# Performance work log

Hardware: AMD Instinct MI355X
Metric: run time of the kernel (lower is better)

## Reference

```python
import jax, jax.numpy as jnp
import numpy as np

INPUT_DIM = 512
KEY_DIM = 256
VOCAB = 10000
MAX_LEN = 300


def setup_inputs() -> dict:
    key = jax.random.key(0)
    ks = jax.random.split(key, 20)
    s = 0.05
    B, S, D, K, V = 32, 196, INPUT_DIM, KEY_DIM, VOCAB
    inp = {
        'x': jax.random.normal(ks[0], (B, S, D), jnp.float32),
        'emb': jax.random.normal(ks[1], (V, D), jnp.float32) * s,
        'Wk': jax.random.normal(ks[2], (K, D), jnp.float32) * s,
        'bk': jnp.zeros((K,), jnp.float32),
        'Wv': jax.random.normal(ks[3], (K, D), jnp.float32) * s,
        'bv': jnp.zeros((K,), jnp.float32),
        'Wq': jax.random.normal(ks[4], (K, D), jnp.float32) * s,
        'bq': jnp.zeros((K,), jnp.float32),
        'Wp': jax.random.normal(ks[5], (V, D + K), jnp.float32) * s,
        'bp': jnp.zeros((V,), jnp.float32),
        # LSTM cell 0: input = concat(embed, context) -> D + K
        'Wih0': jax.random.normal(ks[6], (4 * D, D + K), jnp.float32) * s,
        'Whh0': jax.random.normal(ks[7], (4 * D, D), jnp.float32) * s,
        'bih0': jnp.zeros((4 * D,), jnp.float32),
        'bhh0': jnp.zeros((4 * D,), jnp.float32),
        # LSTM cell 1: input = hidden of cell 0 -> D
        'Wih1': jax.random.normal(ks[8], (4 * D, D), jnp.float32) * s,
        'Whh1': jax.random.normal(ks[9], (4 * D, D), jnp.float32) * s,
        'bih1': jnp.zeros((4 * D,), jnp.float32),
        'bhh1': jnp.zeros((4 * D,), jnp.float32),
    }
    return inp


def _lstm_cell(inp, h, c, Wih, Whh, bih, bhh):
    # torch LSTMCell gate order: i, f, g, o
    gates = inp @ Wih.T + bih + h @ Whh.T + bhh
    i, f, g, o = jnp.split(gates, 4, axis=-1)
    c_new = jax.nn.sigmoid(f) * c + jax.nn.sigmoid(i) * jnp.tanh(g)
    h_new = jax.nn.sigmoid(o) * jnp.tanh(c_new)
    return h_new, c_new


def reference(x, emb, Wk, bk, Wv, bv, Wq, bq, Wp, bp,
              Wih0, Whh0, bih0, bhh0, Wih1, Whh1, bih1, bhh1):
    B = x.shape[0]
    D = Whh0.shape[1]
    K = Wk.shape[0]
    scale = 1.0 / jnp.sqrt(jnp.asarray(K, x.dtype))
    keys = x @ Wk.T + bk      # (B, S, K)
    values = x @ Wv.T + bv    # (B, S, K)

    tok0 = jnp.zeros((B,), jnp.int32)           # argmax of zeros(B,1) == 0
    ctx0 = jnp.zeros((B, K), x.dtype)
    h0 = jnp.zeros((B, D), x.dtype)
    c0 = jnp.zeros((B, D), x.dtype)
    h1 = jnp.zeros((B, D), x.dtype)
    c1 = jnp.zeros((B, D), x.dtype)

    def step(carry, _):
        tok, ctx, h0, c0, h1, c1 = carry
        embed = jnp.concatenate([emb[tok], ctx], axis=1)   # (B, D+K)
        h0, c0 = _lstm_cell(embed, h0, c0, Wih0, Whh0, bih0, bhh0)
        h1, c1 = _lstm_cell(h0, h1, c1, Wih1, Whh1, bih1, bhh1)
        q = h1 @ Wq.T + bq                                  # (B, K)
        energy = jnp.einsum('bsk,bk->bs', keys, q) * scale  # (B, S)
        attn = jax.nn.softmax(energy, axis=-1)
        ctx = jnp.einsum('bs,bsk->bk', attn, values)        # (B, K)
        out = jnp.concatenate([h1, ctx], axis=1)            # (B, D+K)
        pred = out @ Wp.T + bp                              # (B, V)
        tok = jnp.argmax(pred, axis=-1).astype(jnp.int32)
        return (tok, ctx, h0, c0, h1, c1), pred

    _, preds = jax.lax.scan(step, (tok0, ctx0, h0, c0, h1, c1), None, length=MAX_LEN)
    return jnp.transpose(preds, (1, 0, 2))  # (B, MAX_LEN, V)
```

## Files before the change

kernel.cpp:

```cpp
#include <hip/hip_runtime.h>
#include <math.h>


typedef unsigned long long u64;

#define NS 196
#define ND 512
#define NK 256
#define NV 10000
#define NT 300
#define NBLK 256
#define NTHR 512
#define NPRED 209
#define ATT0 224
#define SCOPE __HIP_MEMORY_SCOPE_AGENT

__device__ __forceinline__ float sigm(float x) { return 1.0f / (1.0f + expf(-x)); }

__device__ __forceinline__ float aldf(const float* p) {
  return __hip_atomic_load(p, __ATOMIC_RELAXED, SCOPE);
}
__device__ __forceinline__ void astf(float* p, float v) {
  __hip_atomic_store(p, v, __ATOMIC_RELAXED, SCOPE);
}
__device__ __forceinline__ u64 aldu(const u64* p) {
  return __hip_atomic_load(p, __ATOMIC_RELAXED, SCOPE);
}
__device__ __forceinline__ void astu(u64* p, u64 v) {
  __hip_atomic_store(p, v, __ATOMIC_RELAXED, SCOPE);
}

__device__ __forceinline__ u64 packmax(float x, int v) {
  unsigned u = __float_as_uint(x);
  u = (u & 0x80000000u) ? ~u : (u | 0x80000000u);
  return ((u64)u << 32) | (u64)(0xFFFFFFFFu - (unsigned)v);
}

__device__ __forceinline__ int eslot(int b, int k4) {
  return b * 32 + ((k4 & ~7) | ((k4 ^ b) & 7));
}

__device__ __forceinline__ void gbar(unsigned* bar, int bid, unsigned ep, bool fenced) {
  __syncthreads();
  if (threadIdx.x == 0) {
    if (fenced) __threadfence();
    asm volatile("s_waitcnt vmcnt(0)" ::: "memory");
    const int g = bid & 7;
    const unsigned old = __hip_atomic_fetch_add(&bar[g * 32], 1u, __ATOMIC_RELAXED, SCOPE);
    if (old == ep * 32u - 1u) {
      const unsigned r = __hip_atomic_fetch_add(&bar[512], 1u, __ATOMIC_RELAXED, SCOPE);
      if (r == ep * 8u - 1u) {
#pragma unroll
        for (int i = 0; i < 8; ++i)
          __hip_atomic_store(&bar[256 + i * 32], ep, __ATOMIC_RELAXED, SCOPE);
      }
    }
    while (__hip_atomic_load(&bar[256 + g * 32], __ATOMIC_RELAXED, SCOPE) < ep)
      __builtin_amdgcn_s_sleep(1);
    if (fenced) __threadfence();
  }
  __syncthreads();
}

__global__ __launch_bounds__(256) void k_zbar(unsigned* bar) {
  const int i = blockIdx.x * 256 + threadIdx.x;
  if (i < 1024) bar[i] = 0u;
}

struct Params {
  const float *x, *emb, *Wk, *bk, *Wv, *bv, *Wq, *bq, *Wp, *bp;
  const float *Wih0, *Whh0, *bih0, *bhh0, *Wih1, *Whh1, *bih1, *bhh1;
  float *out, *keys, *values, *h0t, *h1t, *c0, *c1, *ctx;
  u64 *amax;
  unsigned *bar;
};

__global__ __launch_bounds__(NTHR, 1) void k_all(Params p) {
  extern __shared__ float dyn[];
  float* W0lds = dyn;
  float* W1lds = dyn + 10240;
  float* stage = dyn + 18432;

  __shared__ __align__(16) float arena[2560];
  __shared__ int tok_lds[32];
  __shared__ u64 cand2[32][12];

  const int bid = blockIdx.x;
  const int t = threadIdx.x;
  const int lane = t & 63;
  const int w = t >> 6;

#define GP(ks, r, b)  arena[((ks) * 8 + (r)) * 32 + (b)]
#define GS(r, b)      arena[1024 + (r) * 32 + (b)]

  {
    const int g = bid * NTHR + t;
    if (g < 65536) astf(&p.h0t[g], 0.0f);
    if (g < 8192) astf(&p.ctx[g], 0.0f);
    if (g < 256) astu(&p.amax[g], (g < 32) ? ((1ull << 32) | 0xFFFFFFFFull) : 0ull);
  }
  if (t < 64) {
    const int idx = (bid * 2 + (t >> 5)) * 32 + (t & 31);
    p.c0[idx] = 0.0f;
    p.c1[idx] = 0.0f;
  }
  {
    const int r = t >> 6, ln = t & 63;
    const int grow = (r >> 1) * ND + bid * 2 + (r & 1);
    const float* s0i = p.Wih0 + (size_t)grow * 768;
    const float* s0h = p.Whh0 + (size_t)grow * ND;
#pragma unroll
    for (int j = 0; j < 5; ++j) {
      const int col = 4 * (ln + 64 * j);
      const float4 v = (col < 768) ? *(const float4*)(s0i + col)
                                   : *(const float4*)(s0h + (col - 768));
      *(float4*)(W0lds + r * 1280 + col) = v;
    }
    const float* s1i = p.Wih1 + (size_t)grow * ND;
    const float* s1h = p.Whh1 + (size_t)grow * ND;
#pragma unroll
    for (int j = 0; j < 4; ++j) {
      const int col = 4 * (ln + 64 * j);
      const float4 v = (col < 512) ? *(const float4*)(s1i + col)
                                   : *(const float4*)(s1h + (col - 512));
      *(float4*)(W1lds + r * 1024 + col) = v;
    }
  }
  {
    const int kc = bid & 7, bb = bid >> 3;
    const int kl = t & 31, sg = t >> 5;
    const int k = kc * 32 + kl;
    float ak[13], av[13];
#pragma unroll
    for (int i = 0; i < 13; ++i) { ak[i] = 0.f; av[i] = 0.f; }
    const float* wkr = p.Wk + (size_t)k * ND;
    const float* wvr = p.Wv + (size_t)k * ND;
    const float* xb = p.x + (size_t)bb * NS * ND;
    for (int j = 0; j < ND; j += 4) {
      const float4 wk4 = *(const float4*)(wkr + j);
      const float4 wv4 = *(const float4*)(wvr + j);
#pragma unroll
      for (int si = 0; si < 13; ++si) {
        const int s = sg + si * 16;
        if (s < NS) {
          const float4 xv = *(const float4*)(xb + (size_t)s * ND + j);
          ak[si] += wk4.x * xv.x + wk4.y * xv.y + wk4.z * xv.z + wk4.w * xv.w;
          av[si] += wv4.x * xv.x + wv4.y * xv.y + wv4.z * xv.z + wv4.w * xv.w;
        }
      }
    }
    const float bkk = p.bk[k], bvv = p.bv[k];
#pragma unroll
    for (int si = 0; si < 13; ++si) {
      const int s = sg + si * 16;
      if (s < NS) {
        const size_t o = ((size_t)bb * NS + s) * NK + k;
        p.keys[o] = ak[si] + bkk;
        p.values[o] = av[si] + bvv;
      }
    }
  }
  unsigned ep = 1;
  gbar(p.bar, bid, ep++, true);

  for (int step = 0; step < NT; ++step) {
    const int cur = step & 1;
    const float* h0c = p.h0t + cur * 16384;
    float* h0n = p.h0t + (cur ^ 1) * 16384;
    const float* h1c = p.h1t + cur * 16384;
    float* h1n = p.h1t + (cur ^ 1) * 16384;

    if (t < 32) {
      u64 m = aldu(&p.amax[t]);
#pragma unroll
      for (int s2 = 1; s2 < 8; ++s2) { const u64 o = aldu(&p.amax[s2 * 32 + t]); if (o > m) m = o; }
      tok_lds[t] = (int)(0xFFFFFFFFu - (unsigned)(m & 0xFFFFFFFFull));
    }
    __syncthreads();
    {
      const int rq = w >> 2, ks = w & 3;
      const int b = lane & 31, kq = lane >> 5;
      const int s8 = ks * 2 + kq;
      const int rb = rq * 4;
      float a0 = 0.f, a1 = 0.f, a2 = 0.f, a3 = 0.f;
      for (int c = 0; c < 4; ++c) {
        {
          const int eb = t >> 4, sl = t & 15;
          const float* er = p.emb + (size_t)tok_lds[eb] * ND + c * 128;
          *(float4*)(stage + 4 * eslot(eb, sl)) = *(const float4*)(er + 4 * sl);
          *(float4*)(stage + 4 * eslot(eb, sl + 16)) = *(const float4*)(er + 4 * (sl + 16));
        }
        __syncthreads();
#pragma unroll
        for (int jj = 0; jj < 4; ++jj) {
          const int f4 = ks * 8 + kq * 4 + jj;
          const float4 a4 = *(const float4*)(stage + 4 * eslot(b, f4));
          const int wc = c * 128 + 4 * f4;
          const float4 q0 = *(const float4*)(W0lds + (rb + 0) * 1280 + wc);
          const float4 q1 = *(const float4*)(W0lds + (rb + 1) * 1280 + wc);
          const float4 q2 = *(const float4*)(W0lds + (rb + 2) * 1280 + wc);
          const float4 q3 = *(const float4*)(W0lds + (rb + 3) * 1280 + wc);
          a0 += q0.x * a4.x + q0.y * a4.y + q0.z * a4.z + q0.w * a4.w;
          a1 += q1.x * a4.x + q1.y * a4.y + q1.z * a4.z + q1.w * a4.w;
          a2 += q2.x * a4.x + q2.y * a4.y + q2.z * a4.z + q2.w * a4.w;
          a3 += q3.x * a4.x + q3.y * a4.y + q3.z * a4.z + q3.w * a4.w;
        }
        __syncthreads();
      }
#pragma unroll 4
      for (int j = 0; j < 8; ++j) {
        const int k0 = (s8 * 8 + j) * 4;
        float4 x4;
        x4.x = aldf(p.ctx + (k0 + 0) * 32 + b);
        x4.y = aldf(p.ctx + (k0 + 1) * 32 + b);
        x4.z = aldf(p.ctx + (k0 + 2) * 32 + b);
        x4.w = aldf(p.ctx + (k0 + 3) * 32 + b);
        const int wc = 512 + k0;
        const float4 q0 = *(const float4*)(W0lds + (rb + 0) * 1280 + wc);
        const float4 q1 = *(const float4*)(W0lds + (rb + 1) * 1280 + wc);
        const float4 q2 = *(const float4*)(W0lds + (rb + 2) * 1280 + wc);
        const float4 q3 = *(const float4*)(W0lds + (rb + 3) * 1280 + wc);
        a0 += q0.x * x4.x + q0.y * x4.y + q0.z * x4.z + q0.w * x4.w;
        a1 += q1.x * x4.x + q1.y * x4.y + q1.z * x4.z + q1.w * x4.w;
        a2 += q2.x * x4.x + q2.y * x4.y + q2.z * x4.z + q2.w * x4.w;
        a3 += q3.x * x4.x + q3.y * x4.y + q3.z * x4.z + q3.w * x4.w;
      }
#pragma unroll 4
      for (int j = 0; j < 16; ++j) {
        const int k0 = (s8 * 16 + j) * 4;
        float4 x4;
        x4.x = aldf(h0c + (k0 + 0) * 32 + b);
        x4.y = aldf(h0c + (k0 + 1) * 32 + b);
        x4.z = aldf(h0c + (k0 + 2) * 32 + b);
        x4.w = aldf(h0c + (k0 + 3) * 32 + b);
        const int wc = 768 + k0;
        const float4 q0 = *(const float4*)(W0lds + (rb + 0) * 1280 + wc);
        const float4 q1 = *(const float4*)(W0lds + (rb + 1) * 1280 + wc);
        const float4 q2 = *(const float4*)(W0lds + (rb + 2) * 1280 + wc);
        const float4 q3 = *(const float4*)(W0lds + (rb + 3) * 1280 + wc);
        a0 += q0.x * x4.x + q0.y * x4.y + q0.z * x4.z + q0.w * x4.w;
        a1 += q1.x * x4.x + q1.y * x4.y + q1.z * x4.z + q1.w * x4.w;
        a2 += q2.x * x4.x + q2.y * x4.y + q2.z * x4.z + q2.w * x4.w;
        a3 += q3.x * x4.x + q3.y * x4.y + q3.z * x4.z + q3.w * x4.w;
      }
      a0 += __shfl_xor(a0, 32);
      a1 += __shfl_xor(a1, 32);
      a2 += __shfl_xor(a2, 32);
      a3 += __shfl_xor(a3, 32);
      if (kq == 0) {
        GP(ks, rb + 0, b) = a0; GP(ks, rb + 1, b) = a1;
        GP(ks, rb + 2, b) = a2; GP(ks, rb + 3, b) = a3;
      }
    }
    __syncthreads();
    if (t < 256) {
      const int r = t >> 5, b2 = t & 31;
      const int grow = (r >> 1) * ND + bid * 2 + (r & 1);
      GS(r, b2) = GP(0, r, b2) + GP(1, r, b2) + GP(2, r, b2) + GP(3, r, b2)
                + p.bih0[grow] + p.bhh0[grow];
    }
    __syncthreads();
    if (t < 64) {
      const int dl = t >> 5, b2 = t & 31;
      const int idx = (bid * 2 + dl) * 32 + b2;
      const float gi = GS(0 + dl, b2), gf = GS(2 + dl, b2);
      const float gg = GS(4 + dl, b2), go = GS(6 + dl, b2);
      const float cn = sigm(gf) * p.c0[idx] + sigm(gi) * tanhf(gg);
      p.c0[idx] = cn;
      astf(&h0n[idx], sigm(go) * tanhf(cn));
    }
    gbar(p.bar, bid, ep++, false);

    if (bid == 0 && t < 256) astu(&p.amax[t], 0ull);
    {
      const int rq = w >> 2, ks = w & 3;
      const int b = lane & 31, kq = lane >> 5;
      const int s8 = ks * 2 + kq;
      const int rb = rq * 4;
      float a0 = 0.f, a1 = 0.f, a2 = 0.f, a3 = 0.f;
#pragma unroll 4
      for (int j = 0; j < 32; ++j) {
        const int k0 = s8 * 128 + j * 4;
        const float* src = (k0 < 512) ? (h0n + k0 * 32) : (h1c + (k0 - 512) * 32);
        float4 x4;
        x4.x = aldf(src + 0 * 32 + b);
        x4.y = aldf(src + 1 * 32 + b);
        x4.z = aldf(src + 2 * 32 + b);
        x4.w = aldf(src + 3 * 32 + b);
        const float4 q0 = *(const float4*)(W1lds + (rb + 0) * 1024 + k0);
        const float4 q1 = *(const float4*)(W1lds + (rb + 1) * 1024 + k0);
        const float4 q2 = *(const float4*)(W1lds + (rb + 2) * 1024 + k0);
        const float4 q3 = *(const float4*)(W1lds + (rb + 3) * 1024 + k0);
        a0 += q0.x * x4.x + q0.y * x4.y + q0.z * x4.z + q0.w * x4.w;
        a1 += q1.x * x4.x + q1.y * x4.y + q1.z * x4.z + q1.w * x4.w;
        a2 += q2.x * x4.x + q2.y * x4.y + q2.z * x4.z + q2.w * x4.w;
        a3 += q3.x * x4.x + q3.y * x4.y + q3.z * x4.z + q3.w * x4.w;
      }
      a0 += __shfl_xor(a0, 32);
      a1 += __shfl_xor(a1, 32);
      a2 += __shfl_xor(a2, 32);
      a3 += __shfl_xor(a3, 32);
      if (kq == 0) {
        GP(ks, rb + 0, b) = a0; GP(ks, rb + 1, b) = a1;
        GP(ks, rb + 2, b) = a2; GP(ks, rb + 3, b) = a3;
      }
    }
    __syncthreads();
    if (t < 256) {
      const int r = t >> 5, b2 = t & 31;
      const int grow = (r >> 1) * ND + bid * 2 + (r & 1);
      GS(r, b2) = GP(0, r, b2) + GP(1, r, b2) + GP(2, r, b2) + GP(3, r, b2)
                + p.bih1[grow] + p.bhh1[grow];
    }
    __syncthreads();
    if (t < 64) {
      const int dl = t >> 5, b2 = t & 31;
      const int idx = (bid * 2 + dl) * 32 + b2;
      const float gi = GS(0 + dl, b2), gf = GS(2 + dl, b2);
      const float gg = GS(4 + dl, b2), go = GS(6 + dl, b2);
      const float cn = sigm(gf) * p.c1[idx] + sigm(gi) * tanhf(gg);
      p.c1[idx] = cn;
      astf(&h1n[idx], sigm(go) * tanhf(cn));
    }
    gbar(p.bar, bid, ep++, false);

    float acc[6];
#pragma unroll
    for (int r = 0; r < 6; ++r) acc[r] = 0.f;
    if (bid >= ATT0) {
      const int b = bid - ATT0;
      float* hb  = arena;
      float* qs  = arena + 512;
      float* red = arena + 768;
      float* smx = arena + 1024;
      hb[t] = aldf(h1n + t * 32 + b);
      __syncthreads();
      const int kl = lane & 31, rh = lane >> 5;
      for (int pp = 0; pp < 16; ++pp) {
        const int r = w * 32 + pp * 2 + rh;
        const float* wq = p.Wq + (size_t)r * ND + kl * 4;
        float a = 0.f;
#pragma unroll
        for (int i = 0; i < 4; ++i) {
          const float4 w4 = *(const float4*)(wq + i * 128);
          const float4 h4 = *(const float4*)(hb + i * 128 + kl * 4);
          a += w4.x * h4.x + w4.y * h4.y + w4.z * h4.z + w4.w * h4.w;
        }
#pragma unroll
        for (int mk = 1; mk < 32; mk <<= 1) a += __shfl_xor(a, mk);
        if (kl == 0) qs[r] = (a + p.bq[r]) * 0.0625f;
      }
      __syncthreads();
      for (int pp = 0; pp < 13; ++pp) {
        const int s = pp * 16 + w * 2 + rh;
        float a = 0.f;
        if (s < NS) {
          const float* kr = p.keys + ((size_t)b * NS + s) * NK + kl * 4;
#pragma unroll
          for (int i = 0; i < 2; ++i) {
            const float4 k4 = *(const float4*)(kr + i * 128);
            const float4 q4 = *(const float4*)(qs + i * 128 + kl * 4);
            a += k4.x * q4.x + k4.y * q4.y + k4.z * q4.z + k4.w * q4.w;
          }
        }
#pragma unroll
        for (int mk = 1; mk < 32; mk <<= 1) a += __shfl_xor(a, mk);
        if (kl == 0 && s < NS) smx[s] = a;
      }
      __syncthreads();
      float e = -INFINITY;
      if (t < 256) { e = (t < NS) ? smx[t] : -INFINITY; red[t] = e; }
      __syncthreads();
      for (int off = 128; off; off >>= 1) {
        if (t < off) red[t] = fmaxf(red[t], red[t + off]);
        __syncthreads();
      }
      const float mx = red[0];
      __syncthreads();
      float a = 0.f;
      if (t < 256) { a = (t < NS) ? expf(e - mx) : 0.f; red[t] = a; }
      __syncthreads();
      for (int off = 128; off; off >>= 1) {
        if (t < off) red[t] += red[t + off];
        __syncthreads();
      }
      const float inv = 1.0f / red[0];
      if (t < 256) smx[t] = a * inv;
      __syncthreads();
      if (t < 256) {
        const float* vb = p.values + (size_t)b * NS * NK + t;
        float c0_ = 0.f, c1_ = 0.f, c2_ = 0.f, c3_ = 0.f;
        for (int s = 0; s < NS; s += 4) {
          c0_ += smx[s + 0] * vb[(size_t)(s + 0) * NK];
          c1_ += smx[s + 1] * vb[(size_t)(s + 1) * NK];
          c2_ += smx[s + 2] * vb[(size_t)(s + 2) * NK];
          c3_ += smx[s + 3] * vb[(size_t)(s + 3) * NK];
        }
        astf(&p.ctx[t * 32 + b], (c0_ + c1_) + (c2_ + c3_));
      }
    } else if (bid < NPRED) {
      const int b = lane & 31, kq = lane >> 5;
      const int rbase = bid * 48 + w * 6;
      int rc[6];
#pragma unroll
      for (int r = 0; r < 6; ++r) rc[r] = (rbase + r < NV) ? (rbase + r) : (NV - 1);
#pragma unroll 2
      for (int j = 0; j < 64; ++j) {
        const int k0 = kq * 256 + j * 4;
        float4 x4;
        x4.x = aldf(h1n + (k0 + 0) * 32 + b);
        x4.y = aldf(h1n + (k0 + 1) * 32 + b);
        x4.z = aldf(h1n + (k0 + 2) * 32 + b);
        x4.w = aldf(h1n + (k0 + 3) * 32 + b);
#pragma unroll
        for (int r = 0; r < 6; ++r) {
          const float4 w4 = *(const float4*)(p.Wp + (size_t)rc[r] * 768 + k0);
          acc[r] += w4.x * x4.x + w4.y * x4.y + w4.z * x4.z + w4.w * x4.w;
        }
      }
    }
    gbar(p.bar, bid, ep++, false);

    if (bid < NPRED) {
      const int b = lane & 31, kq = lane >> 5;
      const int rbase = bid * 48 + w * 6;
      int rc[6];
#pragma unroll
      for (int r = 0; r < 6; ++r) rc[r] = (rbase + r < NV) ? (rbase + r) : (NV - 1);
#pragma unroll 2
      for (int j = 0; j < 32; ++j) {
        const int kc_ = kq * 128 + j * 4;
        float4 x4;
        x4.x = aldf(p.ctx + (kc_ + 0) * 32 + b);
        x4.y = aldf(p.ctx + (kc_ + 1) * 32 + b);
        x4.z = aldf(p.ctx + (kc_ + 2) * 32 + b);
        x4.w = aldf(p.ctx + (kc_ + 3) * 32 + b);
#pragma unroll
        for (int r = 0; r < 6; ++r) {
          const float4 w4 = *(const float4*)(p.Wp + (size_t)rc[r] * 768 + 512 + kc_);
          acc[r] += w4.x * x4.x + w4.y * x4.y + w4.z * x4.z + w4.w * x4.w;
        }
      }
#pragma unroll
      for (int r = 0; r < 6; ++r) acc[r] += __shfl_xor(acc[r], 32);
      if (kq == 0) {
#pragma unroll
        for (int r = 0; r < 6; ++r)
          arena[(w * 6 + r) * 32 + b] = acc[r];
      }
      __syncthreads();
      if (t < 384) {
        const int b2 = t & 31, rg = t >> 5;
        const int vb = bid * 48 + rg * 4;
        u64 m = 0ull;
        if (vb + 3 < NV) {
          float4 v;
          float* vp = &v.x;
#pragma unroll
          for (int i = 0; i < 4; ++i) {
            const int row = rg * 4 + i;
            vp[i] = arena[row * 32 + b2] + p.bp[vb + i];
          }
          *(float4*)(p.out + ((size_t)b2 * NT + step) * NV + vb) = v;
          m = packmax(v.x, vb + 0);
          const u64 o1 = packmax(v.y, vb + 1); if (o1 > m) m = o1;
          const u64 o2 = packmax(v.z, vb + 2); if (o2 > m) m = o2;
          const u64 o3 = packmax(v.w, vb + 3); if (o3 > m) m = o3;
        }
        cand2[b2][rg] = m;
      }
      __syncthreads();
      if (t < 32) {
        u64 mm = cand2[t][0];
#pragma unroll
        for (int i = 1; i < 12; ++i) { const u64 o = cand2[t][i]; if (o > mm) mm = o; }
        (void)__hip_atomic_fetch_max(&p.amax[(bid & 7) * 32 + t], mm, __ATOMIC_RELAXED, SCOPE);
      }
    }
    gbar(p.bar, bid, ep++, false);
  }
#undef GP
#undef GS
}

extern "C" void kernel_launch(void* const* d_in, const int* in_sizes, int n_in,
                              void* d_out, int out_size, void* d_ws, size_t ws_size,
                              hipStream_t stream) {
  (void)in_sizes; (void)n_in; (void)out_size; (void)ws_size;
  Params prm;
  prm.x    = (const float*)d_in[0];
  prm.emb  = (const float*)d_in[1];
  prm.Wk   = (const float*)d_in[2];
  prm.bk   = (const float*)d_in[3];
  prm.Wv   = (const float*)d_in[4];
  prm.bv   = (const float*)d_in[5];
  prm.Wq   = (const float*)d_in[6];
  prm.bq   = (const float*)d_in[7];
  prm.Wp   = (const float*)d_in[8];
  prm.bp   = (const float*)d_in[9];
  prm.Wih0 = (const float*)d_in[10];
  prm.Whh0 = (const float*)d_in[11];
  prm.bih0 = (const float*)d_in[12];
  prm.bhh0 = (const float*)d_in[13];
  prm.Wih1 = (const float*)d_in[14];
  prm.Whh1 = (const float*)d_in[15];
  prm.bih1 = (const float*)d_in[16];
  prm.bhh1 = (const float*)d_in[17];
  prm.out  = (float*)d_out;

  float* ws = (float*)d_ws;
  prm.keys   = ws;
  prm.values = prm.keys + 1605632;
  prm.h0t    = prm.values + 1605632;
  prm.h1t    = prm.h0t + 32768;
  prm.c0     = prm.h1t + 32768;
  prm.c1     = prm.c0 + 16384;
  prm.ctx    = prm.c1 + 16384;
  prm.amax   = (u64*)(prm.ctx + 8192);
  prm.bar    = (unsigned*)(prm.amax + 256);

  const int LDS = (10240 + 8192 + 4096) * 4;
  (void)hipFuncSetAttribute((const void*)k_all, hipFuncAttributeMaxDynamicSharedMemorySize, LDS);

  k_zbar<<<4, 256, 0, stream>>>(prm.bar);
  void* args[] = { &prm };
  (void)hipLaunchCooperativeKernel((const void*)k_all, dim3(NBLK), dim3(NTHR), args,
                                   (unsigned)LDS, stream);
}
```

Baseline: 24.84 ms.

## Vectorize recurrent-state loads with batch-major lane mapping in LSTM and projection matvecs

Remaps the threads of the LSTM0 ctx/h0 matvec, the LSTM1 matvec and the output projection so each lane loads four consecutive batch entries as one 16-byte volatile vector load. This replaces the scalar per-element atomic loads of the shared hidden and context state. Each lane now keeps v4f accumulators over four batches, and a three-level shuffle-xor reduction runs across the k-slices. The split of the LSTM0 work changes as well: the ctx/h0 part gets its own partial-sum region in the arena. In return the code needs more shuffles and more accumulator registers, and relies on volatile loads for visibility between blocks.

```diff
diff --git a/kernel.cpp b/kernel.cpp
--- a/kernel.cpp
+++ b/kernel.cpp
@@ -3,6 +3,7 @@
 
 
 typedef unsigned long long u64;
+typedef float v4f __attribute__((ext_vector_type(4)));
 
 #define NS 196
 #define ND 512
@@ -29,6 +30,9 @@
 __device__ __forceinline__ void astu(u64* p, u64 v) {
   __hip_atomic_store(p, v, __ATOMIC_RELAXED, SCOPE);
 }
+__device__ __forceinline__ v4f vald4(const float* p) {
+  return *(const volatile v4f*)p;
+}
 
 __device__ __forceinline__ u64 packmax(float x, int v) {
   unsigned u = __float_as_uint(x);
@@ -89,9 +93,6 @@
   const int t = threadIdx.x;
   const int lane = t & 63;
   const int w = t >> 6;
-
-#define GP(ks, r, b)  arena[((ks) * 8 + (r)) * 32 + (b)]
-#define GS(r, b)      arena[1024 + (r) * 32 + (b)]
 
   {
     const int g = bid * NTHR + t;
@@ -180,7 +181,6 @@
     {
       const int rq = w >> 2, ks = w & 3;
       const int b = lane & 31, kq = lane >> 5;
-      const int s8 = ks * 2 + kq;
       const int rb = rq * 4;
       float a0 = 0.f, a1 = 0.f, a2 = 0.f, a3 = 0.f;
       for (int c = 0; c < 4; ++c) {
@@ -207,64 +207,70 @@
         }
         __syncthreads();
       }
-#pragma unroll 4
-      for (int j = 0; j < 8; ++j) {
-        const int k0 = (s8 * 8 + j) * 4;
-        float4 x4;
-        x4.x = aldf(p.ctx + (k0 + 0) * 32 + b);
-        x4.y = aldf(p.ctx + (k0 + 1) * 32 + b);
-        x4.z = aldf(p.ctx + (k0 + 2) * 32 + b);
-        x4.w = aldf(p.ctx + (k0 + 3) * 32 + b);
-        const int wc = 512 + k0;
-        const float4 q0 = *(const float4*)(W0lds + (rb + 0) * 1280 + wc);
-        const float4 q1 = *(const float4*)(W0lds + (rb + 1) * 1280 + wc);
-        const float4 q2 = *(const float4*)(W0lds + (rb + 2) * 1280 + wc);
-        const float4 q3 = *(const float4*)(W0lds + (rb + 3) * 1280 + wc);
-        a0 += q0.x * x4.x + q0.y * x4.y + q0.z * x4.z + q0.w * x4.w;
-        a1 += q1.x * x4.x + q1.y * x4.y + q1.z * x4.z + q1.w * x4.w;
-        a2 += q2.x * x4.x + q2.y * x4.y + q2.z * x4.z + q2.w * x4.w;
-        a3 += q3.x * x4.x + q3.y * x4.y + q3.z * x4.z + q3.w * x4.w;
-      }
-#pragma unroll 4
-      for (int j = 0; j < 16; ++j) {
-        const int k0 = (s8 * 16 + j) * 4;
-        float4 x4;
-        x4.x = aldf(h0c + (k0 + 0) * 32 + b);
-        x4.y = aldf(h0c + (k0 + 1) * 32 + b);
-        x4.z = aldf(h0c + (k0 + 2) * 32 + b);
-        x4.w = aldf(h0c + (k0 + 3) * 32 + b);
-        const int wc = 768 + k0;
-        const float4 q0 = *(const float4*)(W0lds + (rb + 0) * 1280 + wc);
-        const float4 q1 = *(const float4*)(W0lds + (rb + 1) * 1280 + wc);
-        const float4 q2 = *(const float4*)(W0lds + (rb + 2) * 1280 + wc);
-        const float4 q3 = *(const float4*)(W0lds + (rb + 3) * 1280 + wc);
-        a0 += q0.x * x4.x + q0.y * x4.y + q0.z * x4.z + q0.w * x4.w;
-        a1 += q1.x * x4.x + q1.y * x4.y + q1.z * x4.z + q1.w * x4.w;
-        a2 += q2.x * x4.x + q2.y * x4.y + q2.z * x4.z + q2.w * x4.w;
-        a3 += q3.x * x4.x + q3.y * x4.y + q3.z * x4.z + q3.w * x4.w;
-      }
       a0 += __shfl_xor(a0, 32);
       a1 += __shfl_xor(a1, 32);
       a2 += __shfl_xor(a2, 32);
       a3 += __shfl_xor(a3, 32);
       if (kq == 0) {
-        GP(ks, rb + 0, b) = a0; GP(ks, rb + 1, b) = a1;
-        GP(ks, rb + 2, b) = a2; GP(ks, rb + 3, b) = a3;
+        arena[(ks * 8 + rb + 0) * 32 + b] = a0;
+        arena[(ks * 8 + rb + 1) * 32 + b] = a1;
+        arena[(ks * 8 + rb + 2) * 32 + b] = a2;
+        arena[(ks * 8 + rb + 3) * 32 + b] = a3;
+      }
+    }
+    {
+      const int rq4 = w >> 1, kh = w & 1;
+      const int bq = lane & 7, kl = lane >> 3;
+      const int r0 = rq4 * 2, r1 = r0 + 1;
+      const float* wr0 = W0lds + r0 * 1280 + 512 + kh * 384 + kl * 4;
+      const float* wr1 = W0lds + r1 * 1280 + 512 + kh * 384 + kl * 4;
+      v4f ac0 = {0.f, 0.f, 0.f, 0.f}, ac1 = {0.f, 0.f, 0.f, 0.f};
+#pragma unroll 3
+      for (int j = 0; j < 12; ++j) {
+        const int kk = kh * 384 + j * 32 + kl * 4;
+        const float* asrc = (kk < 256) ? (p.ctx + (size_t)kk * 32)
+                                       : (h0c + (size_t)(kk - 256) * 32);
+        const v4f x0 = vald4(asrc + 0 * 32 + bq * 4);
+        const v4f x1 = vald4(asrc + 1 * 32 + bq * 4);
+        const v4f x2 = vald4(asrc + 2 * 32 + bq * 4);
+        const v4f x3 = vald4(asrc + 3 * 32 + bq * 4);
+        const v4f q0 = *(const v4f*)(wr0 + j * 32);
+        const v4f q1 = *(const v4f*)(wr1 + j * 32);
+        ac0 += q0[0] * x0 + q0[1] * x1 + q0[2] * x2 + q0[3] * x3;
+        ac1 += q1[0] * x0 + q1[1] * x1 + q1[2] * x2 + q1[3] * x3;
+      }
+#pragma unroll
+      for (int c = 0; c < 4; ++c) {
+        float v0 = ac0[c], v1 = ac1[c];
+        v0 += __shfl_xor(v0, 8);  v1 += __shfl_xor(v1, 8);
+        v0 += __shfl_xor(v0, 16); v1 += __shfl_xor(v1, 16);
+        v0 += __shfl_xor(v0, 32); v1 += __shfl_xor(v1, 32);
+        ac0[c] = v0; ac1[c] = v1;
+      }
+      if (kl == 0) {
+#pragma unroll
+        for (int i = 0; i < 4; ++i) {
+          arena[1024 + (kh * 8 + r0) * 32 + bq * 4 + i] = ac0[i];
+          arena[1024 + (kh * 8 + r1) * 32 + bq * 4 + i] = ac1[i];
+        }
       }
     }
     __syncthreads();
     if (t < 256) {
       const int r = t >> 5, b2 = t & 31;
       const int grow = (r >> 1) * ND + bid * 2 + (r & 1);
-      GS(r, b2) = GP(0, r, b2) + GP(1, r, b2) + GP(2, r, b2) + GP(3, r, b2)
-                + p.bih0[grow] + p.bhh0[grow];
+      arena[1536 + r * 32 + b2] =
+          arena[(0 * 8 + r) * 32 + b2] + arena[(1 * 8 + r) * 32 + b2]
+        + arena[(2 * 8 + r) * 32 + b2] + arena[(3 * 8 + r) * 32 + b2]
+        + arena[1024 + (0 * 8 + r) * 32 + b2] + arena[1024 + (1 * 8 + r) * 32 + b2]
+        + p.bih0[grow] + p.bhh0[grow];
     }
     __syncthreads();
     if (t < 64) {
       const int dl = t >> 5, b2 = t & 31;
       const int idx = (bid * 2 + dl) * 32 + b2;
-      const float gi = GS(0 + dl, b2), gf = GS(2 + dl, b2);
-      const float gg = GS(4 + dl, b2), go = GS(6 + dl, b2);
+      const float gi = arena[1536 + (0 + dl) * 32 + b2], gf = arena[1536 + (2 + dl) * 32 + b2];
+      const float gg = arena[1536 + (4 + dl) * 32 + b2], go = arena[1536 + (6 + dl) * 32 + b2];
       const float cn = sigm(gf) * p.c0[idx] + sigm(gi) * tanhf(gg);
       p.c0[idx] = cn;
       astf(&h0n[idx], sigm(go) * tanhf(cn));
@@ -273,60 +279,64 @@
 
     if (bid == 0 && t < 256) astu(&p.amax[t], 0ull);
     {
-      const int rq = w >> 2, ks = w & 3;
-      const int b = lane & 31, kq = lane >> 5;
-      const int s8 = ks * 2 + kq;
-      const int rb = rq * 4;
-      float a0 = 0.f, a1 = 0.f, a2 = 0.f, a3 = 0.f;
+      const int rq4 = w >> 1, kh = w & 1;
+      const int bq = lane & 7, kl = lane >> 3;
+      const int r0 = rq4 * 2, r1 = r0 + 1;
+      const float* wr0 = W1lds + r0 * 1024 + kh * 512 + kl * 4;
+      const float* wr1 = W1lds + r1 * 1024 + kh * 512 + kl * 4;
+      const float* abase = (kh == 0) ? h0n : h1c;
+      v4f ac0 = {0.f, 0.f, 0.f, 0.f}, ac1 = {0.f, 0.f, 0.f, 0.f};
 #pragma unroll 4
-      for (int j = 0; j < 32; ++j) {
-        const int k0 = s8 * 128 + j * 4;
-        const float* src = (k0 < 512) ? (h0n + k0 * 32) : (h1c + (k0 - 512) * 32);
-        float4 x4;
-        x4.x = aldf(src + 0 * 32 + b);
-        x4.y = aldf(src + 1 * 32 + b);
-        x4.z = aldf(src + 2 * 32 + b);
-        x4.w = aldf(src + 3 * 32 + b);
-        const float4 q0 = *(const float4*)(W1lds + (rb + 0) * 1024 + k0);
-        const float4 q1 = *(const float4*)(W1lds + (rb + 1) * 1024 + k0);
-        const float4 q2 = *(const float4*)(W1lds + (rb + 2) * 1024 + k0);
-        const float4 q3 = *(const float4*)(W1lds + (rb + 3) * 1024 + k0);
-        a0 += q0.x * x4.x + q0.y * x4.y + q0.z * x4.z + q0.w * x4.w;
-        a1 += q1.x * x4.x + q1.y * x4.y + q1.z * x4.z + q1.w * x4.w;
-        a2 += q2.x * x4.x + q2.y * x4.y + q2.z * x4.z + q2.w * x4.w;
-        a3 += q3.x * x4.x + q3.y * x4.y + q3.z * x4.z + q3.w * x4.w;
-      }
-      a0 += __shfl_xor(a0, 32);
-      a1 += __shfl_xor(a1, 32);
-      a2 += __shfl_xor(a2, 32);
-      a3 += __shfl_xor(a3, 32);
-      if (kq == 0) {
-        GP(ks, rb + 0, b) = a0; GP(ks, rb + 1, b) = a1;
-        GP(ks, rb + 2, b) = a2; GP(ks, rb + 3, b) = a3;
+      for (int j = 0; j < 16; ++j) {
+        const float* asrc = abase + (size_t)(j * 32 + kl * 4) * 32;
+        const v4f x0 = vald4(asrc + 0 * 32 + bq * 4);
+        const v4f x1 = vald4(asrc + 1 * 32 + bq * 4);
+        const v4f x2 = vald4(asrc + 2 * 32 + bq * 4);
+        const v4f x3 = vald4(asrc + 3 * 32 + bq * 4);
+        const v4f q0 = *(const v4f*)(wr0 + j * 32);
+        const v4f q1 = *(const v4f*)(wr1 + j * 32);
+        ac0 += q0[0] * x0 + q0[1] * x1 + q0[2] * x2 + q0[3] * x3;
+        ac1 += q1[0] * x0 + q1[1] * x1 + q1[2] * x2 + q1[3] * x3;
+      }
+#pragma unroll
+      for (int c = 0; c < 4; ++c) {
+        float v0 = ac0[c], v1 = ac1[c];
+        v0 += __shfl_xor(v0, 8);  v1 += __shfl_xor(v1, 8);
+        v0 += __shfl_xor(v0, 16); v1 += __shfl_xor(v1, 16);
+        v0 += __shfl_xor(v0, 32); v1 += __shfl_xor(v1, 32);
+        ac0[c] = v0; ac1[c] = v1;
+      }
+      if (kl == 0) {
+#pragma unroll
+        for (int i = 0; i < 4; ++i) {
+          arena[(kh * 8 + r0) * 32 + bq * 4 + i] = ac0[i];
+          arena[(kh * 8 + r1) * 32 + bq * 4 + i] = ac1[i];
+        }
       }
     }
     __syncthreads();
     if (t < 256) {
       const int r = t >> 5, b2 = t & 31;
       const int grow = (r >> 1) * ND + bid * 2 + (r & 1);
-      GS(r, b2) = GP(0, r, b2) + GP(1, r, b2) + GP(2, r, b2) + GP(3, r, b2)
-                + p.bih1[grow] + p.bhh1[grow];
+      arena[512 + r * 32 + b2] =
+          arena[(0 * 8 + r) * 32 + b2] + arena[(1 * 8 + r) * 32 + b2]
+        + p.bih1[grow] + p.bhh1[grow];
     }
     __syncthreads();
     if (t < 64) {
       const int dl = t >> 5, b2 = t & 31;
       const int idx = (bid * 2 + dl) * 32 + b2;
-      const float gi = GS(0 + dl, b2), gf = GS(2 + dl, b2);
-      const float gg = GS(4 + dl, b2), go = GS(6 + dl, b2);
+      const float gi = arena[512 + (0 + dl) * 32 + b2], gf = arena[512 + (2 + dl) * 32 + b2];
+      const float gg = arena[512 + (4 + dl) * 32 + b2], go = arena[512 + (6 + dl) * 32 + b2];
       const float cn = sigm(gf) * p.c1[idx] + sigm(gi) * tanhf(gg);
       p.c1[idx] = cn;
       astf(&h1n[idx], sigm(go) * tanhf(cn));
     }
     gbar(p.bar, bid, ep++, false);
 
-    float acc[6];
-#pragma unroll
-    for (int r = 0; r < 6; ++r) acc[r] = 0.f;
+    v4f pa[6];
+#pragma unroll
+    for (int r = 0; r < 6; ++r) pa[r] = (v4f){0.f, 0.f, 0.f, 0.f};
     if (bid >= ATT0) {
       const int b = bid - ATT0;
       float* hb  = arena;
@@ -399,54 +409,65 @@
         astf(&p.ctx[t * 32 + b], (c0_ + c1_) + (c2_ + c3_));
       }
     } else if (bid < NPRED) {
-      const int b = lane & 31, kq = lane >> 5;
+      const int bq = lane & 7, kl = lane >> 3;
       const int rbase = bid * 48 + w * 6;
       int rc[6];
 #pragma unroll
       for (int r = 0; r < 6; ++r) rc[r] = (rbase + r < NV) ? (rbase + r) : (NV - 1);
 #pragma unroll 2
-      for (int j = 0; j < 64; ++j) {
-        const int k0 = kq * 256 + j * 4;
-        float4 x4;
-        x4.x = aldf(h1n + (k0 + 0) * 32 + b);
-        x4.y = aldf(h1n + (k0 + 1) * 32 + b);
-        x4.z = aldf(h1n + (k0 + 2) * 32 + b);
-        x4.w = aldf(h1n + (k0 + 3) * 32 + b);
+      for (int j = 0; j < 16; ++j) {
+        const int kk = j * 32 + kl * 4;
+        const float* asrc = h1n + (size_t)kk * 32;
+        const v4f x0 = vald4(asrc + 0 * 32 + bq * 4);
+        const v4f x1 = vald4(asrc + 1 * 32 + bq * 4);
+        const v4f x2 = vald4(asrc + 2 * 32 + bq * 4);
+        const v4f x3 = vald4(asrc + 3 * 32 + bq * 4);
 #pragma unroll
         for (int r = 0; r < 6; ++r) {
-          const float4 w4 = *(const float4*)(p.Wp + (size_t)rc[r] * 768 + k0);
-          acc[r] += w4.x * x4.x + w4.y * x4.y + w4.z * x4.z + w4.w * x4.w;
+          const v4f q = *(const v4f*)(p.Wp + (size_t)rc[r] * 768 + kk);
+          pa[r] += q[0] * x0 + q[1] * x1 + q[2] * x2 + q[3] * x3;
         }
       }
     }
     gbar(p.bar, bid, ep++, false);
 
     if (bid < NPRED) {
-      const int b = lane & 31, kq = lane >> 5;
+      const int bq = lane & 7, kl = lane >> 3;
       const int rbase = bid * 48 + w * 6;
       int rc[6];
 #pragma unroll
       for (int r = 0; r < 6; ++r) rc[r] = (rbase + r < NV) ? (rbase + r) : (NV - 1);
 #pragma unroll 2
-      for (int j = 0; j < 32; ++j) {
-        const int kc_ = kq * 128 + j * 4;
-        float4 x4;
-        x4.x = aldf(p.ctx + (kc_ + 0) * 32 + b);
-        x4.y = aldf(p.ctx + (kc_ + 1) * 32 + b);
-        x4.z = aldf(p.ctx + (kc_ + 2) * 32 + b);
-        x4.w = aldf(p.ctx + (kc_ + 3) * 32 + b);
+      for (int j = 0; j < 8; ++j) {
+        const int kk = j * 32 + kl * 4;
+        const float* asrc = p.ctx + (size_t)kk * 32;
+        const v4f x0 = vald4(asrc + 0 * 32 + bq * 4);
+        const v4f x1 = vald4(asrc + 1 * 32 + bq * 4);
+        const v4f x2 = vald4(asrc + 2 * 32 + bq * 4);
+        const v4f x3 = vald4(asrc + 3 * 32 + bq * 4);
 #pragma unroll
         for (int r = 0; r < 6; ++r) {
-          const float4 w4 = *(const float4*)(p.Wp + (size_t)rc[r] * 768 + 512 + kc_);
-          acc[r] += w4.x * x4.x + w4.y * x4.y + w4.z * x4.z + w4.w * x4.w;
-        }
-      }
-#pragma unroll
-      for (int r = 0; r < 6; ++r) acc[r] += __shfl_xor(acc[r], 32);
-      if (kq == 0) {
+          const v4f q = *(const v4f*)(p.Wp + (size_t)rc[r] * 768 + 512 + kk);
+          pa[r] += q[0] * x0 + q[1] * x1 + q[2] * x2 + q[3] * x3;
+        }
+      }
+#pragma unroll
+      for (int r = 0; r < 6; ++r) {
+#pragma unroll
+        for (int c = 0; c < 4; ++c) {
+          float v = pa[r][c];
+          v += __shfl_xor(v, 8);
+          v += __shfl_xor(v, 16);
+          v += __shfl_xor(v, 32);
+          pa[r][c] = v;
+        }
+      }
+      if (kl == 0) {
 #pragma unroll
         for (int r = 0; r < 6; ++r)
-          arena[(w * 6 + r) * 32 + b] = acc[r];
+#pragma unroll
+          for (int i = 0; i < 4; ++i)
+            arena[(w * 6 + r) * 32 + bq * 4 + i] = pa[r][i];
       }
       __syncthreads();
       if (t < 384) {
@@ -479,8 +500,6 @@
     }
     gbar(p.bar, bid, ep++, false);
   }
-#undef GP
-#undef GS
 }
 
 extern "C" void kernel_launch(void* const* d_in, const int* in_sizes, int n_in,
```

New measurement: 32.89 ms. 1.32x slower.
